# Kernel tuning notes

Measured on AMD Instinct MI355X. Metric: run time of the kernel, lower is better.

## Reference

```python
import jax, jax.numpy as jnp
import numpy as np

N_PILLARS_X = 512
N_PILLARS_Y = 512
IN_FEATURES = 6
OUT_FEATURES = 64
N_POINTS = 1_000_000
BN_EPS = 1e-5


def setup_inputs() -> dict:
    key = jax.random.key(0)
    k_x, k_idx, k_w, k_b, k_g, k_beta = jax.random.split(key, 6)
    x = jax.random.normal(k_x, (N_POINTS, IN_FEATURES), dtype=jnp.float32)
    indices = jax.random.randint(k_idx, (N_POINTS, 2), 0, N_PILLARS_X, dtype=jnp.int32)
    # Linear params (torch default init: U(-1/sqrt(fan_in), 1/sqrt(fan_in)))
    bound = 1.0 / np.sqrt(IN_FEATURES)
    W = jax.random.uniform(k_w, (OUT_FEATURES, IN_FEATURES), jnp.float32, -bound, bound)
    b = jax.random.uniform(k_b, (OUT_FEATURES,), jnp.float32, -bound, bound)
    # BatchNorm affine params (torch default: gamma=1, beta=0; randomize slightly)
    gamma = jnp.ones((OUT_FEATURES,), jnp.float32) + 0.1 * jax.random.normal(k_g, (OUT_FEATURES,), jnp.float32)
    beta = 0.1 * jax.random.normal(k_beta, (OUT_FEATURES,), jnp.float32)
    return {"x": x, "indices": indices, "W": W, "b": b, "gamma": gamma, "beta": beta}


def reference(x, indices, W, b, gamma, beta):
    # Linear: (N, 6) @ (6, 64) + b -> (N, 64)
    h = x @ W.T + b
    # BatchNorm1d in training mode: batch statistics over the point dimension (biased var)
    mean = jnp.mean(h, axis=0)
    var = jnp.mean(jnp.square(h - mean), axis=0)
    h = (h - mean) * (gamma * jax.lax.rsqrt(var + BN_EPS)) + beta
    # ReLU
    h = jnp.maximum(h, 0.0)
    # Scatter-add each point's feature vector into its pillar cell
    flat_idx = indices[:, 0].astype(jnp.int32) * N_PILLARS_Y + indices[:, 1].astype(jnp.int32)
    grid = jax.ops.segment_sum(h, flat_idx, num_segments=N_PILLARS_X * N_PILLARS_Y)
    return grid.reshape(N_PILLARS_X, N_PILLARS_Y, OUT_FEATURES)
```

## Files before the change

kernel.cpp:

```cpp
#include <hip/hip_runtime.h>
#include <hip/hip_fp16.h>

#define N_PY 512
#define IN_F 6
#define OUT_F 64
#define N_CELLS (512 * 512)
#define NCOARSE 256
#define NBUCKET 4096
#define N_SB (NBUCKET * 4)
#define CHUNK 2048
#define BN_EPS 1e-5


__device__ __forceinline__ unsigned pack2h(float a, float b) {
    __half ha = __float2half_rn(a), hb = __float2half_rn(b);
    unsigned short ua = *reinterpret_cast<unsigned short*>(&ha);
    unsigned short ub = *reinterpret_cast<unsigned short*>(&hb);
    return (unsigned)ua | ((unsigned)ub << 16);
}

__device__ __forceinline__ float2 unpack2h(unsigned u) {
    __half2 h = *reinterpret_cast<__half2*>(&u);
    return __half22float2(h);
}

__global__ void __launch_bounds__(256)
pfn_stats_hist_kernel(const float* __restrict__ x, const int* __restrict__ idx,
                      int n, float* __restrict__ acc, int* __restrict__ histC) {
    __shared__ int lhist[NCOARSE];
    const int tid = blockIdx.x * blockDim.x + threadIdx.x;
    const int stride = gridDim.x * blockDim.x;
    const int npairs = n >> 1;

    for (int k = threadIdx.x; k < NCOARSE; k += 256) lhist[k] = 0;
    __syncthreads();

    float s[27];
#pragma unroll
    for (int k = 0; k < 27; ++k) s[k] = 0.f;

    for (int q = tid; q < npairs; q += stride) {
        const float4* base4 = (const float4*)(x + (size_t)q * 12);
        const float4 a = base4[0];
        const float4 b4 = base4[1];
        const float4 c4 = base4[2];
        const int4 ij2 = ((const int4*)idx)[q];
        const float p0[6] = {a.x, a.y, a.z, a.w, b4.x, b4.y};
        const float p1[6] = {b4.z, b4.w, c4.x, c4.y, c4.z, c4.w};
#pragma unroll
        for (int j = 0; j < 6; ++j) s[j] += p0[j] + p1[j];
        int k = 6;
#pragma unroll
        for (int i = 0; i < 6; ++i)
#pragma unroll
            for (int j = i; j < 6; ++j) {
                s[k] += p0[i] * p0[j] + p1[i] * p1[j];
                ++k;
            }
        atomicAdd(&lhist[(ij2.x * N_PY + ij2.y) >> 10], 1);
        atomicAdd(&lhist[(ij2.z * N_PY + ij2.w) >> 10], 1);
    }
    if ((n & 1) && tid == 0) {
        const float* p = x + (size_t)(n - 1) * 6;
        float v[6];
#pragma unroll
        for (int j = 0; j < 6; ++j) v[j] = p[j];
#pragma unroll
        for (int j = 0; j < 6; ++j) s[j] += v[j];
        int k = 6;
#pragma unroll
        for (int i = 0; i < 6; ++i)
#pragma unroll
            for (int j = i; j < 6; ++j) { s[k] += v[i] * v[j]; ++k; }
        const int2 ij = ((const int2*)idx)[n - 1];
        atomicAdd(&lhist[(ij.x * N_PY + ij.y) >> 10], 1);
    }

#pragma unroll
    for (int off = 32; off > 0; off >>= 1)
#pragma unroll
        for (int k = 0; k < 27; ++k) s[k] += __shfl_down(s[k], off, 64);

    __shared__ float lds[4][27];
    const int wid = threadIdx.x >> 6;
    const int lane = threadIdx.x & 63;
    if (lane == 0)
#pragma unroll
        for (int k = 0; k < 27; ++k) lds[wid][k] = s[k];
    __syncthreads();

    if (threadIdx.x < 27) {
        const int k = threadIdx.x;
        const float v = lds[0][k] + lds[1][k] + lds[2][k] + lds[3][k];
        atomicAdd(&acc[k], v);
    }
    atomicAdd(&histC[threadIdx.x], lhist[threadIdx.x]);
}

__global__ void __launch_bounds__(256)
pfn_scan_finalize_kernel(const int* __restrict__ histC,
                         int* __restrict__ baseC, int* __restrict__ curC,
                         int* __restrict__ S, int n,
                         const float* __restrict__ acc,
                         const float* __restrict__ W,
                         const float* __restrict__ b,
                         const float* __restrict__ gamma,
                         const float* __restrict__ beta,
                         float* __restrict__ Wp, float* __restrict__ bp) {
    const int tid = threadIdx.x;
    const int v = histC[tid];
    __shared__ int sc[256];
    sc[tid] = v;
    __syncthreads();
#pragma unroll
    for (int off = 1; off < 256; off <<= 1) {
        const int add = (tid >= off) ? sc[tid - off] : 0;
        __syncthreads();
        sc[tid] += add;
        __syncthreads();
    }
    const int excl = sc[tid] - v;
    baseC[tid] = excl;
    curC[tid] = excl;
    if (tid == 0) S[N_SB] = n;

    if (tid < 64) {
        const int f = tid;
        double inv_n = 1.0 / (double)n;
        double mx[6];
#pragma unroll
        for (int j = 0; j < 6; ++j) mx[j] = (double)acc[j] * inv_n;
        double C[6][6];
        {
            int k = 0;
            for (int i = 0; i < 6; ++i)
                for (int j = i; j < 6; ++j) {
                    double e = (double)acc[6 + k] * inv_n - mx[i] * mx[j];
                    C[i][j] = e; C[j][i] = e; ++k;
                }
        }
        double w[6];
#pragma unroll
        for (int j = 0; j < 6; ++j) w[j] = (double)W[f * 6 + j];
        double mean_h = (double)b[f];
#pragma unroll
        for (int j = 0; j < 6; ++j) mean_h += w[j] * mx[j];
        double var_h = 0.0;
        for (int i = 0; i < 6; ++i) {
            double tt = 0.0;
            for (int j = 0; j < 6; ++j) tt += C[i][j] * w[j];
            var_h += w[i] * tt;
        }
        double sgn = (double)gamma[f] / sqrt(var_h + BN_EPS);
#pragma unroll
        for (int j = 0; j < 6; ++j) Wp[f * 6 + j] = (float)(w[j] * sgn);
        bp[f] = (float)(((double)b[f] - mean_h) * sgn + (double)beta[f]);
    }
}

__global__ void __launch_bounds__(256)
pfn_passA_kernel(const float* __restrict__ x, const int* __restrict__ idx,
                 int* __restrict__ curC, uint4* __restrict__ rec, int n) {
    __shared__ int lhist[NCOARSE];
    __shared__ int lbase[NCOARSE];
    __shared__ int lcur[NCOARSE];
    __shared__ int gbase[NCOARSE];
    __shared__ int sc[256];
    __shared__ uint4 stg[CHUNK];

    const int tid = threadIdx.x;
    const int chunkStart = blockIdx.x * CHUNK;
    const int chunkCount = min(CHUNK, n - chunkStart);

    lhist[tid] = 0;
    __syncthreads();

    int cellr[8];
    unsigned u0[8], u1[8], u2[8];
#pragma unroll
    for (int r = 0; r < 8; ++r) {
        const int i = r * 256 + tid;
        cellr[r] = -1;
        if (i < chunkCount) {
            const int p = chunkStart + i;
            const int2 ij = ((const int2*)idx)[p];
            const int cell = ij.x * N_PY + ij.y;
            cellr[r] = cell;
            const float2* xp = (const float2*)(x + (size_t)p * 6);
            const float2 a = xp[0], b2 = xp[1], c = xp[2];
            u0[r] = pack2h(a.x, a.y);
            u1[r] = pack2h(b2.x, b2.y);
            u2[r] = pack2h(c.x, c.y);
            atomicAdd(&lhist[cell >> 10], 1);
        }
    }
    __syncthreads();

    const int v = lhist[tid];
    sc[tid] = v;
    __syncthreads();
#pragma unroll
    for (int off = 1; off < 256; off <<= 1) {
        const int add = (tid >= off) ? sc[tid - off] : 0;
        __syncthreads();
        sc[tid] += add;
        __syncthreads();
    }
    const int excl = sc[tid] - v;
    lbase[tid] = excl;
    lcur[tid] = excl;
    gbase[tid] = (v > 0) ? atomicAdd(&curC[tid], v) : 0;
    __syncthreads();

#pragma unroll
    for (int r = 0; r < 8; ++r) {
        const int cell = cellr[r];
        if (cell >= 0) {
            const int slot = atomicAdd(&lcur[cell >> 10], 1);
            stg[slot] = uint4{u0[r], u1[r], u2[r], (unsigned)cell};
        }
    }
    __syncthreads();

#pragma unroll
    for (int r = 0; r < 8; ++r) {
        const int slot = r * 256 + tid;
        if (slot < chunkCount) {
            const uint4 q = stg[slot];
            const int bkt = (int)(q.w >> 10);
            const int dst = gbase[bkt] + (slot - lbase[bkt]);
            rec[dst] = q;
        }
    }
}

__global__ void __launch_bounds__(256)
pfn_passB_kernel(const uint4* __restrict__ rec, uint4* __restrict__ rec2,
                 const int* __restrict__ baseC, const int* __restrict__ histC,
                 int* __restrict__ S) {
    __shared__ int lh[64];
    __shared__ int lb[64];
    __shared__ int lc[64];
    const int tid = threadIdx.x;
    const int c = blockIdx.x;
    const int segbase = baseC[c];
    const int cnt = histC[c];

    if (tid < 64) lh[tid] = 0;
    __syncthreads();

    for (int i = tid; i < cnt; i += 256) {
        const uint4 q = rec[segbase + i];
        const int fine = (int)((((q.w >> 6) & 15) << 2) | (q.w & 3));
        atomicAdd(&lh[fine], 1);
    }
    __syncthreads();

    if (tid < 64) {
        const int v = lh[tid];
        int incl = v;
#pragma unroll
        for (int off = 1; off < 64; off <<= 1) {
            const int t2 = __shfl_up(incl, off, 64);
            if (tid >= off) incl += t2;
        }
        const int excl = incl - v;
        lb[tid] = excl;
        lc[tid] = excl;
        S[c * 64 + tid] = segbase + excl;
    }
    __syncthreads();

    for (int i = tid; i < cnt; i += 256) {
        const uint4 q = rec[segbase + i];
        const int fine = (int)((((q.w >> 6) & 15) << 2) | (q.w & 3));
        const int off = atomicAdd(&lc[fine], 1);
        rec2[segbase + off] = q;
    }
}

__global__ void __launch_bounds__(256)
pfn_tile_kernel(const uint4* __restrict__ rec2, const int* __restrict__ S,
                const float* __restrict__ Wp, const float* __restrict__ bp,
                float* __restrict__ out) {
    __shared__ float tile[64 * OUT_F];
    __shared__ uint4 stage[4][64];
    const int tid = threadIdx.x;
    const int lane = tid & 63;
    const int wid = tid >> 6;
    const int bucket = blockIdx.x;

    float4* t4 = (float4*)tile;
#pragma unroll
    for (int i = 0; i < 4; ++i)
        t4[tid + 256 * i] = float4{0.f, 0.f, 0.f, 0.f};

    const float w0 = Wp[lane * 6 + 0];
    const float w1 = Wp[lane * 6 + 1];
    const float w2 = Wp[lane * 6 + 2];
    const float w3 = Wp[lane * 6 + 3];
    const float w4 = Wp[lane * 6 + 4];
    const float w5 = Wp[lane * 6 + 5];
    const float bb = bp[lane];

    __syncthreads();

    const int sb = (bucket << 2) | wid;
    const int r0 = S[sb];
    const int cnt = S[sb + 1] - r0;
    uint4* stg = stage[wid];

    for (int chunk = 0; chunk < cnt; chunk += 64) {
        const int m = min(64, cnt - chunk);
        const uint4* src = rec2 + (size_t)(r0 + chunk);
        if (lane < m) stg[lane] = src[lane];
#pragma unroll 4
        for (int j = 0; j < m; ++j) {
            const uint4 q = stg[j];
            const float2 f01 = unpack2h(q.x);
            const float2 f23 = unpack2h(q.y);
            const float2 f45 = unpack2h(q.z);
            float v = bb;
            v = fmaf(w0, f01.x, v); v = fmaf(w1, f01.y, v);
            v = fmaf(w2, f23.x, v); v = fmaf(w3, f23.y, v);
            v = fmaf(w4, f45.x, v); v = fmaf(w5, f45.y, v);
            tile[(((int)q.w & 63) << 6) | lane] += fmaxf(v, 0.f);
        }
    }
    __syncthreads();

    float4* o4 = (float4*)(out + (size_t)bucket * (64 * OUT_F));
#pragma unroll
    for (int i = 0; i < 4; ++i)
        o4[tid + 256 * i] = t4[tid + 256 * i];
}

__global__ void __launch_bounds__(256)
pfn_build_kernel(const int* __restrict__ idx, int n,
                 int* __restrict__ head, int* __restrict__ nxt) {
    const int p = blockIdx.x * blockDim.x + threadIdx.x;
    if (p >= n) return;
    const int2 ij = ((const int2*)idx)[p];
    const int cell = ij.x * N_PY + ij.y;
    nxt[p] = atomicExch(&head[cell], p);
}

__global__ void pfn_finalize_kernel(const float* __restrict__ acc,
                                    const float* __restrict__ W,
                                    const float* __restrict__ b,
                                    const float* __restrict__ gamma,
                                    const float* __restrict__ beta,
                                    int n,
                                    float* __restrict__ Wp,
                                    float* __restrict__ bp) {
    int f = threadIdx.x;
    double inv_n = 1.0 / (double)n;
    double mx[6];
#pragma unroll
    for (int j = 0; j < 6; ++j) mx[j] = (double)acc[j] * inv_n;
    double C[6][6];
    {
        int k = 0;
        for (int i = 0; i < 6; ++i)
            for (int j = i; j < 6; ++j) {
                double e = (double)acc[6 + k] * inv_n - mx[i] * mx[j];
                C[i][j] = e; C[j][i] = e; ++k;
            }
    }
    double w[6];
#pragma unroll
    for (int j = 0; j < 6; ++j) w[j] = (double)W[f * 6 + j];
    double mean_h = (double)b[f];
#pragma unroll
    for (int j = 0; j < 6; ++j) mean_h += w[j] * mx[j];
    double var_h = 0.0;
    for (int i = 0; i < 6; ++i) {
        double t = 0.0;
        for (int j = 0; j < 6; ++j) t += C[i][j] * w[j];
        var_h += w[i] * t;
    }
    double s = (double)gamma[f] / sqrt(var_h + BN_EPS);
#pragma unroll
    for (int j = 0; j < 6; ++j) Wp[f * 6 + j] = (float)(w[j] * s);
    bp[f] = (float)(((double)b[f] - mean_h) * s + (double)beta[f]);
}

__global__ void __launch_bounds__(256)
pfn_output_kernel(const float* __restrict__ x,
                  const int* __restrict__ head,
                  const int* __restrict__ nxt,
                  const float* __restrict__ Wp,
                  const float* __restrict__ bp,
                  float* __restrict__ out) {
    const int lane = threadIdx.x & 63;
    const int cell = __builtin_amdgcn_readfirstlane(
        (int)((blockIdx.x * blockDim.x + threadIdx.x) >> 6));

    const float w0 = Wp[lane * 6 + 0];
    const float w1 = Wp[lane * 6 + 1];
    const float w2 = Wp[lane * 6 + 2];
    const float w3 = Wp[lane * 6 + 3];
    const float w4 = Wp[lane * 6 + 4];
    const float w5 = Wp[lane * 6 + 5];
    const float bb = bp[lane];

    float s = 0.f;
    int p = head[cell];
    while (p >= 0) {
        const float* xp = x + (size_t)p * 6;
        const int pn = nxt[p];
        float v = bb;
        v = fmaf(w0, xp[0], v);
        v = fmaf(w1, xp[1], v);
        v = fmaf(w2, xp[2], v);
        v = fmaf(w3, xp[3], v);
        v = fmaf(w4, xp[4], v);
        v = fmaf(w5, xp[5], v);
        s += fmaxf(v, 0.0f);
        p = pn;
    }
    out[(size_t)cell * OUT_F + lane] = s;
}

extern "C" void kernel_launch(void* const* d_in, const int* in_sizes, int n_in,
                              void* d_out, int out_size, void* d_ws, size_t ws_size,
                              hipStream_t stream) {
    const float* x     = (const float*)d_in[0];
    const int*   idx   = (const int*)d_in[1];
    const float* W     = (const float*)d_in[2];
    const float* b     = (const float*)d_in[3];
    const float* gamma = (const float*)d_in[4];
    const float* beta  = (const float*)d_in[5];
    float* out = (float*)d_out;

    const int n = in_sizes[0] / IN_F;

    float* acc = (float*)d_ws;
    float* Wp  = (float*)((char*)d_ws + 512);
    float* bp  = Wp + OUT_F * IN_F;

    int*   histC = (int*)((char*)d_ws + 4096);
    int*   baseC = (int*)((char*)d_ws + 5120);
    int*   curC  = (int*)((char*)d_ws + 6144);
    int*   S     = (int*)((char*)d_ws + 7168);
    uint4* rec   = (uint4*)((char*)d_ws + 73728);
    uint4* rec2  = rec + n;

    const size_t need = 73728 + (size_t)n * 32;

    if (ws_size >= need) {
        hipMemsetAsync(d_ws, 0, 5120, stream);
        pfn_stats_hist_kernel<<<1024, 256, 0, stream>>>(x, idx, n, acc, histC);
        pfn_scan_finalize_kernel<<<1, 256, 0, stream>>>(
            histC, baseC, curC, S, n, acc, W, b, gamma, beta, Wp, bp);
        pfn_passA_kernel<<<(n + CHUNK - 1) / CHUNK, 256, 0, stream>>>(
            x, idx, curC, rec, n);
        pfn_passB_kernel<<<NCOARSE, 256, 0, stream>>>(rec, rec2, baseC, histC, S);
        pfn_tile_kernel<<<NBUCKET, 256, 0, stream>>>(rec2, S, Wp, bp, out);
    } else {
        int* head = (int*)((char*)d_ws + 4096);
        int* nxt  = head + N_CELLS;
        hipMemsetAsync(d_ws, 0, 5120, stream);
        pfn_stats_hist_kernel<<<1024, 256, 0, stream>>>(x, idx, n, acc, histC);
        hipMemsetAsync(head, 0xFF, (size_t)N_CELLS * sizeof(int), stream);
        pfn_finalize_kernel<<<1, 64, 0, stream>>>(acc, W, b, gamma, beta, n, Wp, bp);
        pfn_build_kernel<<<(n + 255) / 256, 256, 0, stream>>>(idx, n, head, nxt);
        pfn_output_kernel<<<N_CELLS / 4, 256, 0, stream>>>(x, head, nxt, Wp, bp, out);
    }
}
```

Baseline: 102.0 us.

## Move moment accumulation into passA and BN finalize into passB

The first pass now only builds the coarse histogram from indices, so it no longer reads x. The 27 moment sums are instead accumulated in passA, which already loads every point's features, and the BN weight folding moves into block 0 of passB. This removes one full read of x (24 MB) and shrinks the hist kernel's grid. In exchange passA carries 27 more registers and does extra reductions, and block 0 of passB does serial double-precision work.

```diff
diff --git a/kernel.cpp b/kernel.cpp
--- a/kernel.cpp
+++ b/kernel.cpp
@@ -25,88 +25,32 @@
 }
 
 __global__ void __launch_bounds__(256)
-pfn_stats_hist_kernel(const float* __restrict__ x, const int* __restrict__ idx,
-                      int n, float* __restrict__ acc, int* __restrict__ histC) {
+pfn_hist_kernel(const int* __restrict__ idx, int n, int* __restrict__ histC) {
     __shared__ int lhist[NCOARSE];
     const int tid = blockIdx.x * blockDim.x + threadIdx.x;
     const int stride = gridDim.x * blockDim.x;
     const int npairs = n >> 1;
 
-    for (int k = threadIdx.x; k < NCOARSE; k += 256) lhist[k] = 0;
-    __syncthreads();
-
-    float s[27];
-#pragma unroll
-    for (int k = 0; k < 27; ++k) s[k] = 0.f;
+    lhist[threadIdx.x] = 0;
+    __syncthreads();
 
     for (int q = tid; q < npairs; q += stride) {
-        const float4* base4 = (const float4*)(x + (size_t)q * 12);
-        const float4 a = base4[0];
-        const float4 b4 = base4[1];
-        const float4 c4 = base4[2];
         const int4 ij2 = ((const int4*)idx)[q];
-        const float p0[6] = {a.x, a.y, a.z, a.w, b4.x, b4.y};
-        const float p1[6] = {b4.z, b4.w, c4.x, c4.y, c4.z, c4.w};
-#pragma unroll
-        for (int j = 0; j < 6; ++j) s[j] += p0[j] + p1[j];
-        int k = 6;
-#pragma unroll
-        for (int i = 0; i < 6; ++i)
-#pragma unroll
-            for (int j = i; j < 6; ++j) {
-                s[k] += p0[i] * p0[j] + p1[i] * p1[j];
-                ++k;
-            }
         atomicAdd(&lhist[(ij2.x * N_PY + ij2.y) >> 10], 1);
         atomicAdd(&lhist[(ij2.z * N_PY + ij2.w) >> 10], 1);
     }
     if ((n & 1) && tid == 0) {
-        const float* p = x + (size_t)(n - 1) * 6;
-        float v[6];
-#pragma unroll
-        for (int j = 0; j < 6; ++j) v[j] = p[j];
-#pragma unroll
-        for (int j = 0; j < 6; ++j) s[j] += v[j];
-        int k = 6;
-#pragma unroll
-        for (int i = 0; i < 6; ++i)
-#pragma unroll
-            for (int j = i; j < 6; ++j) { s[k] += v[i] * v[j]; ++k; }
         const int2 ij = ((const int2*)idx)[n - 1];
         atomicAdd(&lhist[(ij.x * N_PY + ij.y) >> 10], 1);
     }
-
-#pragma unroll
-    for (int off = 32; off > 0; off >>= 1)
-#pragma unroll
-        for (int k = 0; k < 27; ++k) s[k] += __shfl_down(s[k], off, 64);
-
-    __shared__ float lds[4][27];
-    const int wid = threadIdx.x >> 6;
-    const int lane = threadIdx.x & 63;
-    if (lane == 0)
-#pragma unroll
-        for (int k = 0; k < 27; ++k) lds[wid][k] = s[k];
-    __syncthreads();
-
-    if (threadIdx.x < 27) {
-        const int k = threadIdx.x;
-        const float v = lds[0][k] + lds[1][k] + lds[2][k] + lds[3][k];
-        atomicAdd(&acc[k], v);
-    }
+    __syncthreads();
     atomicAdd(&histC[threadIdx.x], lhist[threadIdx.x]);
 }
 
 __global__ void __launch_bounds__(256)
-pfn_scan_finalize_kernel(const int* __restrict__ histC,
-                         int* __restrict__ baseC, int* __restrict__ curC,
-                         int* __restrict__ S, int n,
-                         const float* __restrict__ acc,
-                         const float* __restrict__ W,
-                         const float* __restrict__ b,
-                         const float* __restrict__ gamma,
-                         const float* __restrict__ beta,
-                         float* __restrict__ Wp, float* __restrict__ bp) {
+pfn_scan_kernel(const int* __restrict__ histC,
+                int* __restrict__ baseC, int* __restrict__ curC,
+                int* __restrict__ S, int n) {
     const int tid = threadIdx.x;
     const int v = histC[tid];
     __shared__ int sc[256];
@@ -123,50 +67,19 @@
     baseC[tid] = excl;
     curC[tid] = excl;
     if (tid == 0) S[N_SB] = n;
-
-    if (tid < 64) {
-        const int f = tid;
-        double inv_n = 1.0 / (double)n;
-        double mx[6];
-#pragma unroll
-        for (int j = 0; j < 6; ++j) mx[j] = (double)acc[j] * inv_n;
-        double C[6][6];
-        {
-            int k = 0;
-            for (int i = 0; i < 6; ++i)
-                for (int j = i; j < 6; ++j) {
-                    double e = (double)acc[6 + k] * inv_n - mx[i] * mx[j];
-                    C[i][j] = e; C[j][i] = e; ++k;
-                }
-        }
-        double w[6];
-#pragma unroll
-        for (int j = 0; j < 6; ++j) w[j] = (double)W[f * 6 + j];
-        double mean_h = (double)b[f];
-#pragma unroll
-        for (int j = 0; j < 6; ++j) mean_h += w[j] * mx[j];
-        double var_h = 0.0;
-        for (int i = 0; i < 6; ++i) {
-            double tt = 0.0;
-            for (int j = 0; j < 6; ++j) tt += C[i][j] * w[j];
-            var_h += w[i] * tt;
-        }
-        double sgn = (double)gamma[f] / sqrt(var_h + BN_EPS);
-#pragma unroll
-        for (int j = 0; j < 6; ++j) Wp[f * 6 + j] = (float)(w[j] * sgn);
-        bp[f] = (float)(((double)b[f] - mean_h) * sgn + (double)beta[f]);
-    }
 }
 
 __global__ void __launch_bounds__(256)
 pfn_passA_kernel(const float* __restrict__ x, const int* __restrict__ idx,
-                 int* __restrict__ curC, uint4* __restrict__ rec, int n) {
+                 int* __restrict__ curC, uint4* __restrict__ rec,
+                 float* __restrict__ acc, int n) {
     __shared__ int lhist[NCOARSE];
     __shared__ int lbase[NCOARSE];
     __shared__ int lcur[NCOARSE];
     __shared__ int gbase[NCOARSE];
     __shared__ int sc[256];
     __shared__ uint4 stg[CHUNK];
+    __shared__ float lmom[4][27];
 
     const int tid = threadIdx.x;
     const int chunkStart = blockIdx.x * CHUNK;
@@ -174,6 +87,10 @@
 
     lhist[tid] = 0;
     __syncthreads();
+
+    float s[27];
+#pragma unroll
+    for (int k = 0; k < 27; ++k) s[k] = 0.f;
 
     int cellr[8];
     unsigned u0[8], u1[8], u2[8];
@@ -188,6 +105,14 @@
             cellr[r] = cell;
             const float2* xp = (const float2*)(x + (size_t)p * 6);
             const float2 a = xp[0], b2 = xp[1], c = xp[2];
+            const float v6[6] = {a.x, a.y, b2.x, b2.y, c.x, c.y};
+#pragma unroll
+            for (int j = 0; j < 6; ++j) s[j] += v6[j];
+            int k = 6;
+#pragma unroll
+            for (int i2 = 0; i2 < 6; ++i2)
+#pragma unroll
+                for (int j = i2; j < 6; ++j) { s[k] += v6[i2] * v6[j]; ++k; }
             u0[r] = pack2h(a.x, a.y);
             u1[r] = pack2h(b2.x, b2.y);
             u2[r] = pack2h(c.x, c.y);
@@ -232,14 +157,34 @@
             rec[dst] = q;
         }
     }
+
+#pragma unroll
+    for (int off = 32; off > 0; off >>= 1)
+#pragma unroll
+        for (int k = 0; k < 27; ++k) s[k] += __shfl_down(s[k], off, 64);
+    const int wid = tid >> 6;
+    const int lane = tid & 63;
+    if (lane == 0)
+#pragma unroll
+        for (int k = 0; k < 27; ++k) lmom[wid][k] = s[k];
+    __syncthreads();
+    if (tid < 27) {
+        const int k = tid;
+        atomicAdd(&acc[k], lmom[0][k] + lmom[1][k] + lmom[2][k] + lmom[3][k]);
+    }
 }
 
 __global__ void __launch_bounds__(256)
 pfn_passB_kernel(const uint4* __restrict__ rec, uint4* __restrict__ rec2,
                  const int* __restrict__ baseC, const int* __restrict__ histC,
-                 int* __restrict__ S) {
+                 int* __restrict__ S, int n,
+                 const float* __restrict__ acc,
+                 const float* __restrict__ W,
+                 const float* __restrict__ b,
+                 const float* __restrict__ gamma,
+                 const float* __restrict__ beta,
+                 float* __restrict__ Wp, float* __restrict__ bp) {
     __shared__ int lh[64];
-    __shared__ int lb[64];
     __shared__ int lc[64];
     const int tid = threadIdx.x;
     const int c = blockIdx.x;
@@ -249,6 +194,39 @@
     if (tid < 64) lh[tid] = 0;
     __syncthreads();
 
+    if (c == 0 && tid < 64) {
+        const int f = tid;
+        double inv_n = 1.0 / (double)n;
+        double mx[6];
+#pragma unroll
+        for (int j = 0; j < 6; ++j) mx[j] = (double)acc[j] * inv_n;
+        double C[6][6];
+        {
+            int k = 0;
+            for (int i = 0; i < 6; ++i)
+                for (int j = i; j < 6; ++j) {
+                    double e = (double)acc[6 + k] * inv_n - mx[i] * mx[j];
+                    C[i][j] = e; C[j][i] = e; ++k;
+                }
+        }
+        double w[6];
+#pragma unroll
+        for (int j = 0; j < 6; ++j) w[j] = (double)W[f * 6 + j];
+        double mean_h = (double)b[f];
+#pragma unroll
+        for (int j = 0; j < 6; ++j) mean_h += w[j] * mx[j];
+        double var_h = 0.0;
+        for (int i = 0; i < 6; ++i) {
+            double tt = 0.0;
+            for (int j = 0; j < 6; ++j) tt += C[i][j] * w[j];
+            var_h += w[i] * tt;
+        }
+        double sgn = (double)gamma[f] / sqrt(var_h + BN_EPS);
+#pragma unroll
+        for (int j = 0; j < 6; ++j) Wp[f * 6 + j] = (float)(w[j] * sgn);
+        bp[f] = (float)(((double)b[f] - mean_h) * sgn + (double)beta[f]);
+    }
+
     for (int i = tid; i < cnt; i += 256) {
         const uint4 q = rec[segbase + i];
         const int fine = (int)((((q.w >> 6) & 15) << 2) | (q.w & 3));
@@ -265,7 +243,6 @@
             if (tid >= off) incl += t2;
         }
         const int excl = incl - v;
-        lb[tid] = excl;
         lc[tid] = excl;
         S[c * 64 + tid] = segbase + excl;
     }
@@ -336,13 +313,64 @@
 }
 
 __global__ void __launch_bounds__(256)
-pfn_build_kernel(const int* __restrict__ idx, int n,
-                 int* __restrict__ head, int* __restrict__ nxt) {
-    const int p = blockIdx.x * blockDim.x + threadIdx.x;
-    if (p >= n) return;
-    const int2 ij = ((const int2*)idx)[p];
-    const int cell = ij.x * N_PY + ij.y;
-    nxt[p] = atomicExch(&head[cell], p);
+pfn_moments_kernel(const float* __restrict__ x, int n, float* __restrict__ acc) {
+    const int tid = blockIdx.x * blockDim.x + threadIdx.x;
+    const int stride = gridDim.x * blockDim.x;
+    const int npairs = n >> 1;
+
+    float s[27];
+#pragma unroll
+    for (int k = 0; k < 27; ++k) s[k] = 0.f;
+
+    for (int q = tid; q < npairs; q += stride) {
+        const float4* base4 = (const float4*)(x + (size_t)q * 12);
+        const float4 a = base4[0];
+        const float4 b4 = base4[1];
+        const float4 c4 = base4[2];
+        const float p0[6] = {a.x, a.y, a.z, a.w, b4.x, b4.y};
+        const float p1[6] = {b4.z, b4.w, c4.x, c4.y, c4.z, c4.w};
+#pragma unroll
+        for (int j = 0; j < 6; ++j) s[j] += p0[j] + p1[j];
+        int k = 6;
+#pragma unroll
+        for (int i = 0; i < 6; ++i)
+#pragma unroll
+            for (int j = i; j < 6; ++j) {
+                s[k] += p0[i] * p0[j] + p1[i] * p1[j];
+                ++k;
+            }
+    }
+    if ((n & 1) && tid == 0) {
+        const float* p = x + (size_t)(n - 1) * 6;
+        float v[6];
+#pragma unroll
+        for (int j = 0; j < 6; ++j) v[j] = p[j];
+#pragma unroll
+        for (int j = 0; j < 6; ++j) s[j] += v[j];
+        int k = 6;
+#pragma unroll
+        for (int i = 0; i < 6; ++i)
+#pragma unroll
+            for (int j = i; j < 6; ++j) { s[k] += v[i] * v[j]; ++k; }
+    }
+
+#pragma unroll
+    for (int off = 32; off > 0; off >>= 1)
+#pragma unroll
+        for (int k = 0; k < 27; ++k) s[k] += __shfl_down(s[k], off, 64);
+
+    __shared__ float lds[4][27];
+    const int wid = threadIdx.x >> 6;
+    const int lane = threadIdx.x & 63;
+    if (lane == 0)
+#pragma unroll
+        for (int k = 0; k < 27; ++k) lds[wid][k] = s[k];
+    __syncthreads();
+
+    if (threadIdx.x < 27) {
+        const int k = threadIdx.x;
+        atomicAdd(&acc[k], lds[0][k] + lds[1][k] + lds[2][k] + lds[3][k]);
+    }
 }
 
 __global__ void pfn_finalize_kernel(const float* __restrict__ acc,
@@ -383,6 +411,16 @@
 #pragma unroll
     for (int j = 0; j < 6; ++j) Wp[f * 6 + j] = (float)(w[j] * s);
     bp[f] = (float)(((double)b[f] - mean_h) * s + (double)beta[f]);
+}
+
+__global__ void __launch_bounds__(256)
+pfn_build_kernel(const int* __restrict__ idx, int n,
+                 int* __restrict__ head, int* __restrict__ nxt) {
+    const int p = blockIdx.x * blockDim.x + threadIdx.x;
+    if (p >= n) return;
+    const int2 ij = ((const int2*)idx)[p];
+    const int cell = ij.x * N_PY + ij.y;
+    nxt[p] = atomicExch(&head[cell], p);
 }
 
 __global__ void __launch_bounds__(256)
@@ -450,18 +488,18 @@
 
     if (ws_size >= need) {
         hipMemsetAsync(d_ws, 0, 5120, stream);
-        pfn_stats_hist_kernel<<<1024, 256, 0, stream>>>(x, idx, n, acc, histC);
-        pfn_scan_finalize_kernel<<<1, 256, 0, stream>>>(
-            histC, baseC, curC, S, n, acc, W, b, gamma, beta, Wp, bp);
+        pfn_hist_kernel<<<256, 256, 0, stream>>>(idx, n, histC);
+        pfn_scan_kernel<<<1, 256, 0, stream>>>(histC, baseC, curC, S, n);
         pfn_passA_kernel<<<(n + CHUNK - 1) / CHUNK, 256, 0, stream>>>(
-            x, idx, curC, rec, n);
-        pfn_passB_kernel<<<NCOARSE, 256, 0, stream>>>(rec, rec2, baseC, histC, S);
+            x, idx, curC, rec, acc, n);
+        pfn_passB_kernel<<<NCOARSE, 256, 0, stream>>>(
+            rec, rec2, baseC, histC, S, n, acc, W, b, gamma, beta, Wp, bp);
         pfn_tile_kernel<<<NBUCKET, 256, 0, stream>>>(rec2, S, Wp, bp, out);
     } else {
         int* head = (int*)((char*)d_ws + 4096);
         int* nxt  = head + N_CELLS;
-        hipMemsetAsync(d_ws, 0, 5120, stream);
-        pfn_stats_hist_kernel<<<1024, 256, 0, stream>>>(x, idx, n, acc, histC);
+        hipMemsetAsync(d_ws, 0, 512, stream);
+        pfn_moments_kernel<<<1024, 256, 0, stream>>>(x, n, acc);
         hipMemsetAsync(head, 0xFF, (size_t)N_CELLS * sizeof(int), stream);
         pfn_finalize_kernel<<<1, 64, 0, stream>>>(acc, W, b, gamma, beta, n, Wp, bp);
         pfn_build_kernel<<<(n + 255) / 256, 256, 0, stream>>>(idx, n, head, nxt);
```

Measured after the change: 86.73 us, median of 3. 14.9% less time.
